# Kernel tuning notes

Hardware: AMD Instinct MI355X
Metric: run time of the kernel (lower is better)

## Reference

```python
import jax, jax.numpy as jnp
import numpy as np

B, C, H, W = 8, 64, 160, 160
N_HEADS = 8
EPS = 1e-6


def conv1x1(x, w, b):
    # x: [B, Cin, H, W], w: [Cout, Cin], b: [Cout]
    return jnp.einsum('oc,bchw->bohw', w, x) + b[None, :, None, None]


def setup_inputs() -> dict:
    key = jax.random.key(0)
    ks = jax.random.split(key, 12)
    s = 0.05
    return {
        'high': jax.random.normal(ks[0], (B, C, H, W), jnp.float32),
        'low': jax.random.normal(ks[1], (B, C, H, W), jnp.float32),
        'wq_high': jax.random.normal(ks[2], (C // 2, C), jnp.float32) * s,
        'bq_high': jnp.zeros((C // 2,), jnp.float32),
        'wq_low': jax.random.normal(ks[3], (C // 2, C), jnp.float32) * s,
        'bq_low': jnp.zeros((C // 2,), jnp.float32),
        'wk': jax.random.normal(ks[4], (C, C), jnp.float32) * s,
        'bk': jnp.zeros((C,), jnp.float32),
        'wv': jax.random.normal(ks[5], (C, C), jnp.float32) * s,
        'bv': jnp.zeros((C,), jnp.float32),
        'wo': jax.random.normal(ks[6], (C, C), jnp.float32) * s,
        'bo': jnp.zeros((C,), jnp.float32),
    }


def reference(high, low, wq_high, bq_high, wq_low, bq_low, wk, bk, wv, bv, wo, bo):
    b, c, h, w = low.shape
    p, d, n = N_HEADS, c // N_HEADS, h * w
    # q branches: [B, C//2, H, W] -> [B, P/2, N, d]
    hq = conv1x1(high, wq_high, bq_high).reshape(b, p // 2, d, n).transpose(0, 1, 3, 2)
    lq = conv1x1(low, wq_low, bq_low).reshape(b, p // 2, d, n).transpose(0, 1, 3, 2)
    q = jax.nn.softplus(jnp.concatenate([hq, lq], axis=1))          # [B, P, N, d]
    k = jax.nn.softplus(conv1x1(low, wk, bk).reshape(b, p, d, n))   # [B, P, d, N]
    v = conv1x1(low, wv, bv).reshape(b, p, d, n)                    # [B, P, d, N]
    # linear-attention context: kT v over spatial N
    attn_map = jnp.einsum('bpmn,bpcn->bpmc', k, v)                  # [B, P, d, d]
    norm = 1.0 / jnp.einsum('bpnc,bpc->bpn', q, jnp.sum(k, axis=-1) + EPS)  # [B, P, N]
    out = jnp.einsum('bpnm,bpmc,bpn->bpcn', q, attn_map, norm)      # [B, P, d, N]
    out = out.reshape(b, c, h, w)
    return conv1x1(out, wo, bo)
```

## Files before the change

kernel.cpp:

```cpp
#include <hip/hip_runtime.h>

#define NPIX  25600
#define NB    8
#define NCH   100
#define CPX   256
#define KCH   200
#define KPX   128
#define EPSV  1e-6f

#define WS_WKVT  0
#define WS_WQT   8192
#define WS_BKV   12288
#define WS_BQ    12416
#define WS_PART  12480
#define WS_G     473280
#define WS_KSE   506048

__device__ __forceinline__ float softplus_(float x) {
  return (x > 20.0f) ? x : __logf(1.0f + __expf(x));
}

template <int CTRL, int RMASK>
__device__ __forceinline__ float dpp_add(float x) {
  int y = __builtin_amdgcn_update_dpp(0, __float_as_int(x), CTRL, RMASK, 0xf, false);
  return x + __int_as_float(y);
}
__device__ __forceinline__ float wave_sum63(float x) {
  x = dpp_add<0x111, 0xf>(x);
  x = dpp_add<0x112, 0xf>(x);
  x = dpp_add<0x114, 0xf>(x);
  x = dpp_add<0x118, 0xf>(x);
  x = dpp_add<0x142, 0xa>(x);
  x = dpp_add<0x143, 0xc>(x);
  return x;
}

__global__ void k0_pack(const float* __restrict__ wq_high, const float* __restrict__ bq_high,
                        const float* __restrict__ wq_low,  const float* __restrict__ bq_low,
                        const float* __restrict__ wk, const float* __restrict__ bk,
                        const float* __restrict__ wv, const float* __restrict__ bv,
                        float* __restrict__ ws) {
  const int tid = threadIdx.x;
  for (int e = tid; e < 8192; e += 256) {
    int j = e & 15, c = (e >> 4) & 63, h = e >> 10, m = j & 7;
    float v = (j < 8) ? wk[(h * 8 + m) * 64 + c] : wv[(h * 8 + m) * 64 + c];
    ws[WS_WKVT + e] = v;
  }
  for (int e = tid; e < 4096; e += 256) {
    int m = e & 7, c = (e >> 3) & 63, h = e >> 9;
    float v = (h < 4) ? wq_high[(h * 8 + m) * 64 + c]
                      : wq_low[((h - 4) * 8 + m) * 64 + c];
    ws[WS_WQT + e] = v;
  }
  for (int e = tid; e < 128; e += 256) {
    int j = e & 15, h = e >> 4, m = j & 7;
    ws[WS_BKV + e] = (j < 8) ? bk[h * 8 + m] : bv[h * 8 + m];
  }
  for (int e = tid; e < 64; e += 256) {
    int m = e & 7, h = e >> 3;
    ws[WS_BQ + e] = (h < 4) ? bq_high[h * 8 + m] : bq_low[(h - 4) * 8 + m];
  }
}

__global__ __attribute__((amdgpu_waves_per_eu(1, 8)))
void k1_kv(const float* __restrict__ low,
           const float* __restrict__ ws,
           float* __restrict__ part) {
  const int b = blockIdx.y >> 1, half = blockIdx.y & 1, chunk = blockIdx.x;
  const int tid = threadIdx.x, lane = tid & 63;
  const int wu = __builtin_amdgcn_readfirstlane(half * 4 + (tid >> 6));
  const float* lowb = low + (size_t)b * 64 * NPIX + chunk * CPX;
  const float* wt = ws + WS_WKVT + wu * 1024;
  const float* bias = ws + WS_BKV + wu * 16;
  float ka[8][4], va[8][4];
#pragma unroll
  for (int m = 0; m < 8; m++) {
    float bkm = bias[m], bvm = bias[8 + m];
#pragma unroll
    for (int px = 0; px < 4; px++) { ka[m][px] = bkm; va[m][px] = bvm; }
  }
#pragma unroll 8
  for (int c = 0; c < 64; c++) {
    float4 x = reinterpret_cast<const float4*>(lowb + (size_t)c * NPIX)[lane];
    const float* wr = wt + c * 16;
#pragma unroll
    for (int m = 0; m < 8; m++) {
      float wkm = wr[m], wvm = wr[8 + m];
      ka[m][0] = fmaf(wkm, x.x, ka[m][0]);
      ka[m][1] = fmaf(wkm, x.y, ka[m][1]);
      ka[m][2] = fmaf(wkm, x.z, ka[m][2]);
      ka[m][3] = fmaf(wkm, x.w, ka[m][3]);
      va[m][0] = fmaf(wvm, x.x, va[m][0]);
      va[m][1] = fmaf(wvm, x.y, va[m][1]);
      va[m][2] = fmaf(wvm, x.z, va[m][2]);
      va[m][3] = fmaf(wvm, x.w, va[m][3]);
    }
  }
#pragma unroll
  for (int m = 0; m < 8; m++)
#pragma unroll
    for (int px = 0; px < 4; px++) ka[m][px] = softplus_(ka[m][px]);
  float* pb = part + ((size_t)(b * 8 + wu) * NCH + chunk) * 72;
#pragma unroll
  for (int m = 0; m < 8; m++) {
    float r[8];
#pragma unroll
    for (int c = 0; c < 8; c++) {
      float a = ka[m][0] * va[c][0];
      a = fmaf(ka[m][1], va[c][1], a);
      a = fmaf(ka[m][2], va[c][2], a);
      r[c] = fmaf(ka[m][3], va[c][3], a);
    }
#pragma unroll
    for (int c = 0; c < 8; c++) r[c] = wave_sum63(r[c]);
    if (lane == 63) {
      reinterpret_cast<float4*>(&pb[m * 8])[0] = make_float4(r[0], r[1], r[2], r[3]);
      reinterpret_cast<float4*>(&pb[m * 8])[1] = make_float4(r[4], r[5], r[6], r[7]);
    }
  }
  {
    float r[8];
#pragma unroll
    for (int m = 0; m < 8; m++)
      r[m] = (ka[m][0] + ka[m][1]) + (ka[m][2] + ka[m][3]);
#pragma unroll
    for (int m = 0; m < 8; m++) r[m] = wave_sum63(r[m]);
    if (lane == 63) {
      reinterpret_cast<float4*>(&pb[64])[0] = make_float4(r[0], r[1], r[2], r[3]);
      reinterpret_cast<float4*>(&pb[64])[1] = make_float4(r[4], r[5], r[6], r[7]);
    }
  }
}

__global__ void k2_g(const float* __restrict__ part, const float* __restrict__ wo,
                     float* __restrict__ ws) {
  const int b = blockIdx.x >> 3, p = blockIdx.x & 7;
  const int tid = threadIdx.x, lane = tid & 63, sub = tid >> 6;
  __shared__ float red[4][72];
  __shared__ float attnL[72];
  const float* src = part + (size_t)(b * 8 + p) * NCH * 72;
  float s0 = 0.0f, s1 = 0.0f;
  for (int ch = sub * (NCH / 4); ch < (sub + 1) * (NCH / 4); ch++) {
    s0 += src[ch * 72 + lane];
    if (lane < 8) s1 += src[ch * 72 + 64 + lane];
  }
  red[sub][lane] = s0;
  if (lane < 8) red[sub][64 + lane] = s1;
  __syncthreads();
  if (tid < 72) attnL[tid] = (red[0][tid] + red[1][tid]) + (red[2][tid] + red[3][tid]);
  __syncthreads();
  if (tid >= 64) {
    if (tid < 72) ws[WS_KSE + (b * 8 + p) * 8 + (tid - 64)] = attnL[tid] + EPSV;
    return;
  }
  const int o = tid;
  float wrow[8];
#pragma unroll
  for (int c = 0; c < 8; c++) wrow[c] = wo[o * 64 + p * 8 + c];
  float* Gp = ws + WS_G + (size_t)(b * 64 + p * 8) * 64;
#pragma unroll
  for (int m = 0; m < 8; m++) {
    float g = 0.0f;
#pragma unroll
    for (int c = 0; c < 8; c++) g = fmaf(attnL[m * 8 + c], wrow[c], g);
    Gp[m * 64 + o] = g;
  }
}

__global__ __attribute__((amdgpu_waves_per_eu(1, 8)))
void k3_main(const float* __restrict__ high,
             const float* __restrict__ low,
             const float* __restrict__ ws,
             const float* __restrict__ bo,
             float* __restrict__ out) {
  const int b = blockIdx.y, chunk = blockIdx.x;
  const int tid = threadIdx.x, lane = tid & 63;
  const int wu = __builtin_amdgcn_readfirstlane(tid >> 6);
  __shared__ float qsL[64 * KPX];
  const float* srcb = ((wu < 4) ? high : low) + (size_t)b * 64 * NPIX + chunk * KPX;
  const float* wq  = ws + WS_WQT + wu * 512;
  const float* bq  = ws + WS_BQ + wu * 8;
  const float* kse = ws + WS_KSE + (b * 8 + wu) * 8;
  const float* Gb  = ws + WS_G + (size_t)b * 4096 + wu * 8;
  float qa[8][2];
#pragma unroll
  for (int m = 0; m < 8; m++) { qa[m][0] = bq[m]; qa[m][1] = bq[m]; }
#pragma unroll 8
  for (int c = 0; c < 64; c++) {
    float2 x = reinterpret_cast<const float2*>(srcb + (size_t)c * NPIX)[lane];
    const float* wr = wq + c * 8;
#pragma unroll
    for (int m = 0; m < 8; m++) {
      float w = wr[m];
      qa[m][0] = fmaf(w, x.x, qa[m][0]);
      qa[m][1] = fmaf(w, x.y, qa[m][1]);
    }
  }
  float s0 = 0.0f, s1 = 0.0f;
#pragma unroll
  for (int m = 0; m < 8; m++) {
    float km = kse[m];
    qa[m][0] = softplus_(qa[m][0]);
    qa[m][1] = softplus_(qa[m][1]);
    s0 = fmaf(qa[m][0], km, s0);
    s1 = fmaf(qa[m][1], km, s1);
  }
  const float r0 = 1.0f / s0, r1 = 1.0f / s1;
#pragma unroll
  for (int m = 0; m < 8; m++) {
    reinterpret_cast<float2*>(&qsL[(wu * 8 + m) * KPX])[lane] =
        make_float2(qa[m][0] * r0, qa[m][1] * r1);
  }
  __syncthreads();
  float acc[8][2];
#pragma unroll
  for (int j = 0; j < 8; j++) { acc[j][0] = bo[wu * 8 + j]; acc[j][1] = acc[j][0]; }
#pragma unroll 8
  for (int pm = 0; pm < 64; pm++) {
    float2 qv = reinterpret_cast<const float2*>(&qsL[pm * KPX])[lane];
    const float* gr = Gb + pm * 64;
#pragma unroll
    for (int j = 0; j < 8; j++) {
      float g = gr[j];
      acc[j][0] = fmaf(g, qv.x, acc[j][0]);
      acc[j][1] = fmaf(g, qv.y, acc[j][1]);
    }
  }
  float* ob = out + (size_t)(b * 64 + wu * 8) * NPIX + chunk * KPX;
#pragma unroll
  for (int j = 0; j < 8; j++) {
    reinterpret_cast<float2*>(ob + (size_t)j * NPIX)[lane] =
        make_float2(acc[j][0], acc[j][1]);
  }
}

extern "C" void kernel_launch(void* const* d_in, const int* in_sizes, int n_in,
                              void* d_out, int out_size, void* d_ws, size_t ws_size,
                              hipStream_t stream) {
  const float* high    = (const float*)d_in[0];
  const float* low     = (const float*)d_in[1];
  const float* wq_high = (const float*)d_in[2];
  const float* bq_high = (const float*)d_in[3];
  const float* wq_low  = (const float*)d_in[4];
  const float* bq_low  = (const float*)d_in[5];
  const float* wk      = (const float*)d_in[6];
  const float* bk      = (const float*)d_in[7];
  const float* wv      = (const float*)d_in[8];
  const float* bv      = (const float*)d_in[9];
  const float* wo      = (const float*)d_in[10];
  const float* bo      = (const float*)d_in[11];
  float* ws  = (float*)d_ws;
  float* out = (float*)d_out;

  k0_pack<<<1, 256, 0, stream>>>(wq_high, bq_high, wq_low, bq_low, wk, bk, wv, bv, ws);
  dim3 grid1(NCH, NB * 2);
  k1_kv<<<grid1, 256, 0, stream>>>(low, ws, ws + WS_PART);
  k2_g<<<64, 256, 0, stream>>>(ws + WS_PART, wo, ws);
  dim3 grid3(KCH, NB);
  k3_main<<<grid3, 512, 0, stream>>>(high, low, ws, bo, out);
}
```

Baseline: 131.0 us.

## Split K and V projection across wave pairs in k1 via LDS exchange

```diff
diff --git a/kernel.cpp b/kernel.cpp
--- a/kernel.cpp
+++ b/kernel.cpp
@@ -66,68 +66,95 @@
 void k1_kv(const float* __restrict__ low,
            const float* __restrict__ ws,
            float* __restrict__ part) {
-  const int b = blockIdx.y >> 1, half = blockIdx.y & 1, chunk = blockIdx.x;
+  const int b = blockIdx.y >> 1, hg = blockIdx.y & 1, chunk = blockIdx.x;
   const int tid = threadIdx.x, lane = tid & 63;
-  const int wu = __builtin_amdgcn_readfirstlane(half * 4 + (tid >> 6));
+  const int wu = __builtin_amdgcn_readfirstlane(tid >> 6);
+  const int hl = wu >> 1, role = wu & 1;
+  const int h = hg * 4 + hl;
+  __shared__ float kvL[4 * 16 * 128];
   const float* lowb = low + (size_t)b * 64 * NPIX + chunk * CPX;
-  const float* wt = ws + WS_WKVT + wu * 1024;
-  const float* bias = ws + WS_BKV + wu * 16;
-  float ka[8][4], va[8][4];
-#pragma unroll
-  for (int m = 0; m < 8; m++) {
-    float bkm = bias[m], bvm = bias[8 + m];
-#pragma unroll
-    for (int px = 0; px < 4; px++) { ka[m][px] = bkm; va[m][px] = bvm; }
-  }
-#pragma unroll 8
-  for (int c = 0; c < 64; c++) {
-    float4 x = reinterpret_cast<const float4*>(lowb + (size_t)c * NPIX)[lane];
-    const float* wr = wt + c * 16;
-#pragma unroll
-    for (int m = 0; m < 8; m++) {
-      float wkm = wr[m], wvm = wr[8 + m];
-      ka[m][0] = fmaf(wkm, x.x, ka[m][0]);
-      ka[m][1] = fmaf(wkm, x.y, ka[m][1]);
-      ka[m][2] = fmaf(wkm, x.z, ka[m][2]);
-      ka[m][3] = fmaf(wkm, x.w, ka[m][3]);
-      va[m][0] = fmaf(wvm, x.x, va[m][0]);
-      va[m][1] = fmaf(wvm, x.y, va[m][1]);
-      va[m][2] = fmaf(wvm, x.z, va[m][2]);
-      va[m][3] = fmaf(wvm, x.w, va[m][3]);
-    }
-  }
-#pragma unroll
-  for (int m = 0; m < 8; m++)
-#pragma unroll
-    for (int px = 0; px < 4; px++) ka[m][px] = softplus_(ka[m][px]);
-  float* pb = part + ((size_t)(b * 8 + wu) * NCH + chunk) * 72;
-#pragma unroll
-  for (int m = 0; m < 8; m++) {
-    float r[8];
-#pragma unroll
-    for (int c = 0; c < 8; c++) {
-      float a = ka[m][0] * va[c][0];
-      a = fmaf(ka[m][1], va[c][1], a);
-      a = fmaf(ka[m][2], va[c][2], a);
-      r[c] = fmaf(ka[m][3], va[c][3], a);
-    }
-#pragma unroll
-    for (int c = 0; c < 8; c++) r[c] = wave_sum63(r[c]);
+  const float* wt = ws + WS_WKVT + h * 1024 + role * 8;
+  const float* bias = ws + WS_BKV + h * 16 + role * 8;
+  float racc[4][8];
+  float ks[8];
+#pragma unroll
+  for (int m = 0; m < 4; m++)
+#pragma unroll
+    for (int c = 0; c < 8; c++) racc[m][c] = 0.0f;
+#pragma unroll
+  for (int m = 0; m < 8; m++) ks[m] = 0.0f;
+  float bias_[8];
+#pragma unroll
+  for (int m = 0; m < 8; m++) bias_[m] = bias[m];
+
+#pragma unroll
+  for (int t = 0; t < 2; t++) {
+    const float* xb = lowb + t * 128;
+    float a[8][2];
+#pragma unroll
+    for (int m = 0; m < 8; m++) { a[m][0] = bias_[m]; a[m][1] = bias_[m]; }
+#pragma unroll 4
+    for (int c = 0; c < 64; c++) {
+      float2 x = reinterpret_cast<const float2*>(xb + (size_t)c * NPIX)[lane];
+      const float* wr = wt + c * 16;
+#pragma unroll
+      for (int m = 0; m < 8; m++) {
+        float w = wr[m];
+        a[m][0] = fmaf(w, x.x, a[m][0]);
+        a[m][1] = fmaf(w, x.y, a[m][1]);
+      }
+    }
+    if (role == 0) {
+#pragma unroll
+      for (int m = 0; m < 8; m++) {
+        a[m][0] = softplus_(a[m][0]);
+        a[m][1] = softplus_(a[m][1]);
+        ks[m] += a[m][0] + a[m][1];
+      }
+    }
+#pragma unroll
+    for (int m = 0; m < 8; m++)
+      reinterpret_cast<float2*>(&kvL[(hl * 16 + role * 8 + m) * 128])[lane] =
+          make_float2(a[m][0], a[m][1]);
+    __syncthreads();
+    if (role == 0) {
+#pragma unroll
+      for (int c = 0; c < 8; c++) {
+        float2 v = reinterpret_cast<const float2*>(&kvL[(hl * 16 + 8 + c) * 128])[lane];
+#pragma unroll
+        for (int m = 0; m < 4; m++)
+          racc[m][c] = fmaf(a[m][1], v.y, fmaf(a[m][0], v.x, racc[m][c]));
+      }
+    } else {
+#pragma unroll
+      for (int m = 0; m < 4; m++) {
+        float2 k = reinterpret_cast<const float2*>(&kvL[(hl * 16 + 4 + m) * 128])[lane];
+#pragma unroll
+        for (int c = 0; c < 8; c++)
+          racc[m][c] = fmaf(k.y, a[c][1], fmaf(k.x, a[c][0], racc[m][c]));
+      }
+    }
+    __syncthreads();
+  }
+  float* pb = part + ((size_t)(b * 8 + h) * NCH + chunk) * 72;
+#pragma unroll
+  for (int m = 0; m < 4; m++) {
+#pragma unroll
+    for (int c = 0; c < 8; c++) racc[m][c] = wave_sum63(racc[m][c]);
     if (lane == 63) {
-      reinterpret_cast<float4*>(&pb[m * 8])[0] = make_float4(r[0], r[1], r[2], r[3]);
-      reinterpret_cast<float4*>(&pb[m * 8])[1] = make_float4(r[4], r[5], r[6], r[7]);
-    }
-  }
-  {
-    float r[8];
-#pragma unroll
-    for (int m = 0; m < 8; m++)
-      r[m] = (ka[m][0] + ka[m][1]) + (ka[m][2] + ka[m][3]);
-#pragma unroll
-    for (int m = 0; m < 8; m++) r[m] = wave_sum63(r[m]);
+      const int row = role == 0 ? m : 4 + m;
+      reinterpret_cast<float4*>(&pb[row * 8])[0] =
+          make_float4(racc[m][0], racc[m][1], racc[m][2], racc[m][3]);
+      reinterpret_cast<float4*>(&pb[row * 8])[1] =
+          make_float4(racc[m][4], racc[m][5], racc[m][6], racc[m][7]);
+    }
+  }
+  if (role == 0) {
+#pragma unroll
+    for (int m = 0; m < 8; m++) ks[m] = wave_sum63(ks[m]);
     if (lane == 63) {
-      reinterpret_cast<float4*>(&pb[64])[0] = make_float4(r[0], r[1], r[2], r[3]);
-      reinterpret_cast<float4*>(&pb[64])[1] = make_float4(r[4], r[5], r[6], r[7]);
+      reinterpret_cast<float4*>(&pb[64])[0] = make_float4(ks[0], ks[1], ks[2], ks[3]);
+      reinterpret_cast<float4*>(&pb[64])[1] = make_float4(ks[4], ks[5], ks[6], ks[7]);
     }
   }
 }
@@ -254,7 +281,7 @@
 
   k0_pack<<<1, 256, 0, stream>>>(wq_high, bq_high, wq_low, bq_low, wk, bk, wv, bv, ws);
   dim3 grid1(NCH, NB * 2);
-  k1_kv<<<grid1, 256, 0, stream>>>(low, ws, ws + WS_PART);
+  k1_kv<<<grid1, 512, 0, stream>>>(low, ws, ws + WS_PART);
   k2_g<<<64, 256, 0, stream>>>(ws + WS_PART, wo, ws);
   dim3 grid3(KCH, NB);
   k3_main<<<grid3, 512, 0, stream>>>(high, low, ws, bo, out);
```

After: 156.4 us. 1.19x slower.
